# Kernel optimization log

Hardware: AMD Instinct MI355X
Metric: run time of the kernel (lower is better)

Reference implementation:

```python
import jax, jax.numpy as jnp
import numpy as np

DIM = 1024
DIM_HEAD = 64
HEADS = 16
BATCH = 2
SEQ = 2048
SCALE = DIM_HEAD ** -0.5


def setup_inputs() -> dict:
    key = jax.random.key(0)
    ks = jax.random.split(key, 5)
    tokens = jax.random.normal(ks[0], (BATCH, SEQ, DIM), dtype=jnp.float32)
    wq = jax.random.normal(ks[1], (HEADS, DIM, DIM_HEAD), dtype=jnp.float32)
    wk = jax.random.normal(ks[2], (HEADS, DIM, DIM_HEAD), dtype=jnp.float32)
    wv = jax.random.normal(ks[3], (HEADS, DIM, DIM_HEAD), dtype=jnp.float32)
    wo = jax.random.normal(ks[4], (HEADS, DIM_HEAD, DIM), dtype=jnp.float32)
    return {"tokens": tokens, "wq": wq, "wk": wk, "wv": wv, "wo": wo}


def reference(tokens, wq, wk, wv, wo):
    # q, k, v: [b, h, n, dh]
    q = jnp.einsum('bnd,hde->bhne', tokens, wq) * SCALE
    k = jnp.einsum('bnd,hde->bhne', tokens, wk)
    v = jnp.einsum('bnd,hde->bhne', tokens, wv)
    sim = jnp.einsum('bhie,bhje->bhij', q, k)          # [b, h, n, n]
    attn = jax.nn.softmax(sim, axis=-1)
    aggregated = jnp.einsum('bhij,bhje->bhie', attn, v)  # [b, h, n, dh]
    retrieved = jnp.einsum('bhne,hed->bnd', aggregated, wo)  # sum over heads
    return retrieved
```

## Files before the change

kernel.cpp:

```cpp
#include <hip/hip_runtime.h>
#include <hip/hip_fp16.h>
#include <stdint.h>

#define BB 2
#define HH 16
#define SS 2048
#define DD 1024
#define DHH 64
#define QSCALE 0.18033688011112042f

typedef _Float16 half8 __attribute__((ext_vector_type(8)));
typedef _Float16 half4 __attribute__((ext_vector_type(4)));
typedef __fp16 fp16x2 __attribute__((ext_vector_type(2)));
typedef float floatx4 __attribute__((ext_vector_type(4)));

__device__ __forceinline__ floatx4 mfma16(half8 a, half8 b, floatx4 c) {
  return __builtin_amdgcn_mfma_f32_16x16x32_f16(a, b, c, 0, 0, 0);
}

__device__ __forceinline__ void dma16(const _Float16* g, _Float16* l) {
  __builtin_amdgcn_global_load_lds(
      (const __attribute__((address_space(1))) uint32_t*)g,
      (__attribute__((address_space(3))) uint32_t*)l,
      16, 0, 0);
}


__global__ __launch_bounds__(256) void convert_kernel(
    const float* __restrict__ wq, const float* __restrict__ wk,
    const float* __restrict__ wv, const float* __restrict__ wo,
    _Float16* __restrict__ Wh, _Float16* __restrict__ Wl,
    _Float16* __restrict__ Wot)
{
  __shared__ float St[64][68];
  const int kt = blockIdx.x;
  const int hy = blockIdx.y;
  const int z  = blockIdx.z;
  const int t  = (int)threadIdx.x;
  const int k0 = kt * 64;

  const float* src = (z == 0) ? (wq + hy * (DD * DHH))
                   : (z == 1) ? (wk + hy * (DD * DHH))
                   : (z == 2) ? (wv + hy * (DD * DHH))
                   : wo;

  const int rr = t >> 4, cc = (t & 15) * 4;
  if (z < 3) {
    #pragma unroll
    for (int i = 0; i < 4; ++i)
      *(floatx4*)&St[rr + 16 * i][cc] =
          *(const floatx4*)(src + (k0 + rr + 16 * i) * DHH + cc);
  } else {
    const int d0 = hy * 64;
    #pragma unroll
    for (int i = 0; i < 4; ++i)
      *(floatx4*)&St[rr + 16 * i][cc] =
          *(const floatx4*)(src + (k0 + rr + 16 * i) * 1024 + d0 + cc);
  }
  __syncthreads();

  const int e = t >> 2, kc = (t & 3) * 16;
  if (z < 3) {
    const int n = z * 1024 + hy * 64 + e;
    half8 hi0, hi1, lo0, lo1;
    #pragma unroll
    for (int u = 0; u < 16; ++u) {
      float x = St[kc + u][e];
      _Float16 hh = (_Float16)x;
      _Float16 ll = (_Float16)(x - (float)hh);
      if (u < 8) { hi0[u] = hh; lo0[u] = ll; }
      else       { hi1[u - 8] = hh; lo1[u - 8] = ll; }
    }
    *(half8*)(Wh + n * 1024 + k0 + kc)     = hi0;
    *(half8*)(Wh + n * 1024 + k0 + kc + 8) = hi1;
    *(half8*)(Wl + n * 1024 + k0 + kc)     = lo0;
    *(half8*)(Wl + n * 1024 + k0 + kc + 8) = lo1;
  } else {
    const int d0 = hy * 64;
    half8 hi0, hi1;
    #pragma unroll
    for (int u = 0; u < 16; ++u) {
      _Float16 hh = (_Float16)St[kc + u][e];
      if (u < 8) hi0[u] = hh; else hi1[u - 8] = hh;
    }
    *(half8*)(Wot + (d0 + e) * 1024 + k0 + kc)     = hi0;
    *(half8*)(Wot + (d0 + e) * 1024 + k0 + kc + 8) = hi1;
  }
}

__global__ __launch_bounds__(256) void tokens_split_kernel(
    const float* __restrict__ tokens,
    _Float16* __restrict__ th, _Float16* __restrict__ tl)
{
  const int i = ((int)blockIdx.x * 256 + (int)threadIdx.x) * 8;
  floatx4 x0 = *(const floatx4*)(tokens + i);
  floatx4 x1 = *(const floatx4*)(tokens + i + 4);
  half8 h, l;
  #pragma unroll
  for (int j = 0; j < 8; ++j) {
    float x = (j < 4) ? x0[j] : x1[j - 4];
    _Float16 hh = (_Float16)x;
    h[j] = hh;
    l[j] = (_Float16)(x - (float)hh);
  }
  *(half8*)(th + i) = h;
  *(half8*)(tl + i) = l;
}

__global__ __launch_bounds__(256) void qkv_gemm_kernel(
    const _Float16* __restrict__ th, const _Float16* __restrict__ tl,
    const _Float16* __restrict__ Wh, const _Float16* __restrict__ Wl,
    _Float16* __restrict__ qh, _Float16* __restrict__ ql,
    _Float16* __restrict__ kh, _Float16* __restrict__ kl,
    _Float16* __restrict__ vt)
{
  __shared__ alignas(16) _Float16 sbuf[2][4][128 * 32];

  const int n0 = blockIdx.x * 128;
  const int m0 = blockIdx.y * 128;
  const int zb = n0 >> 10;
  const bool is_v = (zb == 2);
  const int t = (int)threadIdx.x;
  const int lane = t & 63, wid = t >> 6;
  const int l16 = lane & 15, q4 = lane >> 4;
  const int mw = (wid & 1) * 64, nw = (wid >> 1) * 64;

  const int g  = (lane & 7) ^ ((lane >> 3) & 7);
  const int grow  = (lane >> 3) * 2 + (g >> 2);
  const int gcol8 = (g & 3) * 8;
  const int laneoff = (l16 >> 1) * 128 + (((((l16 & 1) << 2) | q4) ^ (l16 >> 1)) * 16);

  const _Float16* src;
  int arr;
  if (wid == 0)      { src = th + m0 * 1024; arr = 0; }
  else if (wid == 1) { src = Wh + n0 * 1024; arr = 1; }
  else if (wid == 2) { src = Wl + n0 * 1024; arr = 2; }
  else               { src = tl + m0 * 1024; arr = 3; }
  const bool stage_active = !(is_v && wid == 3);
  const _Float16* gsrc = src + grow * 1024 + gcol8;

  const floatx4 z4 = {0.0f, 0.0f, 0.0f, 0.0f};
  floatx4 acc[4][4];
  #pragma unroll
  for (int mi = 0; mi < 4; ++mi)
    #pragma unroll
    for (int ni = 0; ni < 4; ++ni) acc[mi][ni] = z4;

  auto stage = [&](int buf, int kt2) {
    if (stage_active) {
      const _Float16* gp = gsrc + kt2 * 32;
      _Float16* dst = &sbuf[buf][arr][0];
      #pragma unroll
      for (int j = 0; j < 8; ++j)
        dma16(gp + j * 16 * 1024, dst + j * 16 * 32);
    }
  };

  auto compute = [&](int buf) {
    const char* sAh = (const char*)&sbuf[buf][0][0];
    const char* sBh = (const char*)&sbuf[buf][1][0];
    const char* sBl = (const char*)&sbuf[buf][2][0];
    const char* sAl = (const char*)&sbuf[buf][3][0];
    half8 a_h[4];
    #pragma unroll
    for (int mi = 0; mi < 4; ++mi)
      a_h[mi] = *(const half8*)(sAh + (mw + mi * 16) * 64 + laneoff);
    if (!is_v) {
      half8 a_l[4];
      #pragma unroll
      for (int mi = 0; mi < 4; ++mi)
        a_l[mi] = *(const half8*)(sAl + (mw + mi * 16) * 64 + laneoff);
      #pragma unroll
      for (int ni = 0; ni < 4; ++ni) {
        const half8 b_h = *(const half8*)(sBh + (nw + ni * 16) * 64 + laneoff);
        const half8 b_l = *(const half8*)(sBl + (nw + ni * 16) * 64 + laneoff);
        #pragma unroll
        for (int mi = 0; mi < 4; ++mi) {
          acc[mi][ni] = mfma16(a_h[mi], b_h, acc[mi][ni]);
          acc[mi][ni] = mfma16(a_h[mi], b_l, acc[mi][ni]);
          acc[mi][ni] = mfma16(a_l[mi], b_h, acc[mi][ni]);
        }
      }
    } else {
      #pragma unroll
      for (int ni = 0; ni < 4; ++ni) {
        const half8 b_h = *(const half8*)(sBh + (nw + ni * 16) * 64 + laneoff);
        const half8 b_l = *(const half8*)(sBl + (nw + ni * 16) * 64 + laneoff);
        #pragma unroll
        for (int mi = 0; mi < 4; ++mi) {
          acc[mi][ni] = mfma16(a_h[mi], b_h, acc[mi][ni]);
          acc[mi][ni] = mfma16(a_h[mi], b_l, acc[mi][ni]);
        }
      }
    }
  };

  stage(0, 0);
  __syncthreads();

  #pragma unroll 1
  for (int kt = 0; kt < 32; kt += 2) {
    if (kt + 1 < 32) stage(1, kt + 1);
    compute(0);
    __syncthreads();
    if (kt + 2 < 32) stage(0, kt + 2);
    compute(1);
    __syncthreads();
  }

  #pragma unroll
  for (int ni = 0; ni < 4; ++ni) {
    const int ncol = n0 + nw + ni * 16;
    const int h = (ncol >> 6) & 15;
    const int e = (ncol & 63) + l16;
    #pragma unroll
    for (int mi = 0; mi < 4; ++mi) {
      #pragma unroll
      for (int r = 0; r < 4; ++r) {
        const int grow2 = m0 + mw + mi * 16 + q4 * 4 + r;
        const int b = grow2 >> 11, s = grow2 & 2047;
        const float v = acc[mi][ni][r];
        const int qkidx = ((b * HH + h) * SS + s) * DHH + e;
        if (zb == 0) {
          const float vs = v * QSCALE;
          const _Float16 hh = (_Float16)vs;
          qh[qkidx] = hh;
          ql[qkidx] = (_Float16)(vs - (float)hh);
        } else if (zb == 1) {
          const _Float16 hh = (_Float16)v;
          kh[qkidx] = hh;
          kl[qkidx] = (_Float16)(v - (float)hh);
        } else {
          vt[((b * HH + h) * DHH + e) * SS + s] = (_Float16)v;
        }
      }
    }
  }
}

__global__ __launch_bounds__(512) void attn_kernel(
    const _Float16* __restrict__ qh, const _Float16* __restrict__ ql,
    const _Float16* __restrict__ kh, const _Float16* __restrict__ kl,
    const _Float16* __restrict__ vt, _Float16* __restrict__ agg)
{
  __shared__ _Float16 Kh[64][72], Kl[64][72], Vs[64][72];
  __shared__ _Float16 Ps[128][72];

  const int qt = blockIdx.x;
  const int h  = blockIdx.y;
  const int b  = blockIdx.z;
  const int bh = b * HH + h;
  const int t = (int)threadIdx.x;
  const int lane = t & 63, wid = t >> 6;
  const int l16 = lane & 15, q4 = lane >> 4;

  const int sr = t >> 3, sc = (t & 7) * 8;

  half8 qfh[2], qfl[2];
  {
    const int s = qt * 128 + wid * 16 + l16;
    const int base = (bh * SS + s) * DHH + q4 * 8;
    qfh[0] = *(const half8*)(qh + base);
    qfh[1] = *(const half8*)(qh + base + 32);
    qfl[0] = *(const half8*)(ql + base);
    qfl[1] = *(const half8*)(ql + base + 32);
  }

  const floatx4 z4 = {0.0f, 0.0f, 0.0f, 0.0f};
  floatx4 o[4];
  #pragma unroll
  for (int i = 0; i < 4; ++i) o[i] = z4;
  float m_r = -1e30f, l_r = 0.0f;

  half8 pK, pL, pV;
  {
    const int gk = (bh * SS + sr) * DHH + sc;
    pK = *(const half8*)(kh + gk);
    pL = *(const half8*)(kl + gk);
    pV = *(const half8*)(vt + (bh * DHH + sr) * SS + sc);
  }

  for (int kt = 0; kt < 32; ++kt) {
    __syncthreads();
    *(half8*)&Kh[sr][sc] = pK;
    *(half8*)&Kl[sr][sc] = pL;
    *(half8*)&Vs[sr][sc] = pV;
    __syncthreads();

    if (kt < 31) {
      const int k1 = (kt + 1) * 64;
      const int gk = (bh * SS + k1 + sr) * DHH + sc;
      pK = *(const half8*)(kh + gk);
      pL = *(const half8*)(kl + gk);
      pV = *(const half8*)(vt + (bh * DHH + sr) * SS + k1 + sc);
    }

    floatx4 sv[4];
    #pragma unroll
    for (int sub = 0; sub < 4; ++sub) {
      const half8 ah0 = *(const half8*)&Kh[sub * 16 + l16][q4 * 8];
      const half8 ah1 = *(const half8*)&Kh[sub * 16 + l16][q4 * 8 + 32];
      const half8 al0 = *(const half8*)&Kl[sub * 16 + l16][q4 * 8];
      const half8 al1 = *(const half8*)&Kl[sub * 16 + l16][q4 * 8 + 32];
      floatx4 s4 = z4;
      s4 = mfma16(ah0, qfh[0], s4);
      s4 = mfma16(ah1, qfh[1], s4);
      s4 = mfma16(al0, qfh[0], s4);
      s4 = mfma16(al1, qfh[1], s4);
      s4 = mfma16(ah0, qfl[0], s4);
      s4 = mfma16(ah1, qfl[1], s4);
      sv[sub] = s4;
    }

    float mx = fmaxf(fmaxf(sv[0][0], sv[0][1]), fmaxf(sv[0][2], sv[0][3]));
    #pragma unroll
    for (int sub = 1; sub < 4; ++sub)
      mx = fmaxf(mx, fmaxf(fmaxf(sv[sub][0], sv[sub][1]),
                           fmaxf(sv[sub][2], sv[sub][3])));
    mx = fmaxf(mx, __shfl_xor(mx, 16));
    mx = fmaxf(mx, __shfl_xor(mx, 32));
    const float mnew = fmaxf(m_r, mx);

    float psum = 0.0f;
    #pragma unroll
    for (int sub = 0; sub < 4; ++sub) {
      #pragma unroll
      for (int r = 0; r < 4; ++r) {
        float p = exp2f(sv[sub][r] - mnew);
        sv[sub][r] = p;
        psum += p;
      }
    }

    #pragma unroll
    for (int sub = 0; sub < 4; ++sub) {
      fp16x2 p01 = __builtin_amdgcn_cvt_pkrtz(sv[sub][0], sv[sub][1]);
      fp16x2 p23 = __builtin_amdgcn_cvt_pkrtz(sv[sub][2], sv[sub][3]);
      half4 pv;
      pv[0] = (_Float16)p01[0]; pv[1] = (_Float16)p01[1];
      pv[2] = (_Float16)p23[0]; pv[3] = (_Float16)p23[1];
      *(half4*)&Ps[wid * 16 + l16][sub * 16 + q4 * 4] = pv;
    }

    psum += __shfl_xor(psum, 16);
    psum += __shfl_xor(psum, 32);

    if (__any(mnew > m_r)) {
      const float alpha = exp2f(m_r - mnew);
      l_r = l_r * alpha + psum;
      m_r = mnew;
      #pragma unroll
      for (int sub = 0; sub < 4; ++sub)
        #pragma unroll
        for (int r = 0; r < 4; ++r) o[sub][r] *= alpha;
    } else {
      l_r += psum;
    }

    asm volatile("s_waitcnt lgkmcnt(0)" ::: "memory");

    const half8 pb0 = *(const half8*)&Ps[wid * 16 + l16][q4 * 8];
    const half8 pb1 = *(const half8*)&Ps[wid * 16 + l16][q4 * 8 + 32];
    #pragma unroll
    for (int sub = 0; sub < 4; ++sub) {
      const half8 va0 = *(const half8*)&Vs[sub * 16 + l16][q4 * 8];
      const half8 va1 = *(const half8*)&Vs[sub * 16 + l16][q4 * 8 + 32];
      o[sub] = mfma16(va0, pb0, o[sub]);
      o[sub] = mfma16(va1, pb1, o[sub]);
    }
  }

  const float inv = 1.0f / l_r;
  const int s = qt * 128 + wid * 16 + l16;
  #pragma unroll
  for (int sub = 0; sub < 4; ++sub) {
    half4 ov;
    #pragma unroll
    for (int r = 0; r < 4; ++r) ov[r] = (_Float16)(o[sub][r] * inv);
    *(half4*)(agg + (b * SS + s) * (HH * DHH) + h * DHH + sub * 16 + q4 * 4) = ov;
  }
}

__global__ __launch_bounds__(256) void out_gemm_kernel(
    const _Float16* __restrict__ agg, const _Float16* __restrict__ Wot,
    float* __restrict__ out)
{
  __shared__ alignas(16) _Float16 sbuf[2][2][128 * 32];
  const int n0 = blockIdx.x * 128;
  const int m0 = blockIdx.y * 128;
  const int t = (int)threadIdx.x;
  const int lane = t & 63, wid = t >> 6;
  const int l16 = lane & 15, q4 = lane >> 4;
  const int mw = (wid & 1) * 64, nw = (wid >> 1) * 64;

  const int g  = (lane & 7) ^ ((lane >> 3) & 7);
  const int grow  = (lane >> 3) * 2 + (g >> 2);
  const int gcol8 = (g & 3) * 8;
  const int laneoff = (l16 >> 1) * 128 + (((((l16 & 1) << 2) | q4) ^ (l16 >> 1)) * 16);

  const int arr = wid >> 1;
  const int half64 = (wid & 1) * 64;
  const _Float16* src = (arr == 0) ? (agg + m0 * 1024) : (Wot + n0 * 1024);
  const _Float16* gsrc = src + (half64 + grow) * 1024 + gcol8;

  const floatx4 z4 = {0.0f, 0.0f, 0.0f, 0.0f};
  floatx4 acc[4][4];
  #pragma unroll
  for (int mi = 0; mi < 4; ++mi)
    #pragma unroll
    for (int ni = 0; ni < 4; ++ni) acc[mi][ni] = z4;

  auto stage = [&](int buf, int kt2) {
    const _Float16* gp = gsrc + kt2 * 32;
    _Float16* dst = &sbuf[buf][arr][half64 * 32];
    #pragma unroll
    for (int j = 0; j < 4; ++j)
      dma16(gp + j * 16 * 1024, dst + j * 16 * 32);
  };

  auto compute = [&](int buf) {
    const char* sA = (const char*)&sbuf[buf][0][0];
    const char* sB = (const char*)&sbuf[buf][1][0];
    half8 a_f[4];
    #pragma unroll
    for (int mi = 0; mi < 4; ++mi)
      a_f[mi] = *(const half8*)(sA + (mw + mi * 16) * 64 + laneoff);
    #pragma unroll
    for (int ni = 0; ni < 4; ++ni) {
      const half8 b_f = *(const half8*)(sB + (nw + ni * 16) * 64 + laneoff);
      #pragma unroll
      for (int mi = 0; mi < 4; ++mi)
        acc[mi][ni] = mfma16(a_f[mi], b_f, acc[mi][ni]);
    }
  };

  stage(0, 0);
  __syncthreads();

  #pragma unroll 1
  for (int kt = 0; kt < 32; kt += 2) {
    if (kt + 1 < 32) stage(1, kt + 1);
    compute(0);
    __syncthreads();
    if (kt + 2 < 32) stage(0, kt + 2);
    compute(1);
    __syncthreads();
  }

  #pragma unroll
  for (int ni = 0; ni < 4; ++ni)
    #pragma unroll
    for (int mi = 0; mi < 4; ++mi)
      #pragma unroll
      for (int r = 0; r < 4; ++r)
        out[(m0 + mw + mi * 16 + q4 * 4 + r) * 1024 + n0 + nw + ni * 16 + l16] =
            acc[mi][ni][r];
}

extern "C" void kernel_launch(void* const* d_in, const int* in_sizes, int n_in,
                              void* d_out, int out_size, void* d_ws, size_t ws_size,
                              hipStream_t stream)
{
  const float* tokens = (const float*)d_in[0];
  const float* wq = (const float*)d_in[1];
  const float* wk = (const float*)d_in[2];
  const float* wv = (const float*)d_in[3];
  const float* wo = (const float*)d_in[4];
  float* out = (float*)d_out;

  char* ws = (char*)d_ws;
  _Float16* qh  = (_Float16*)(ws);
  _Float16* ql  = (_Float16*)(ws + 8388608);
  _Float16* kh  = (_Float16*)(ws + 16777216);
  _Float16* kl  = (_Float16*)(ws + 25165824);
  _Float16* vt  = (_Float16*)(ws + 33554432);
  _Float16* Wh  = (_Float16*)(ws + 41943040);
  _Float16* Wl  = (_Float16*)(ws + 48234496);
  _Float16* Wot = (_Float16*)(ws + 54525952);
  _Float16* th  = (_Float16*)(ws + 56623104);
  _Float16* tl  = (_Float16*)(ws + 65011712);
  _Float16* agg = (_Float16*)(ws + 56623104);

  convert_kernel<<<dim3(16, 16, 4), 256, 0, stream>>>(wq, wk, wv, wo, Wh, Wl, Wot);
  tokens_split_kernel<<<2048, 256, 0, stream>>>(tokens, th, tl);
  qkv_gemm_kernel<<<dim3(24, 32), 256, 0, stream>>>(th, tl, Wh, Wl, qh, ql, kh, kl, vt);
  attn_kernel<<<dim3(16, 16, 2), 512, 0, stream>>>(qh, ql, kh, kl, vt, agg);
  out_gemm_kernel<<<dim3(8, 32), 256, 0, stream>>>(agg, Wot, out);
}
```

Baseline: 281.0 us.

## Process two query sub-tiles per wave in attention, add lazy rescale and setprio

The attention kernel now runs 256 threads per block, and each wave handles 32 query rows as two 16-row sub-tiles, so each K/V fragment read from LDS feeds twice as many MFMAs. The online-softmax max is updated only when the new max exceeds the running one by more than 8 (in log2 units), which skips most output rescales. MFMA sections are wrapped in s_setprio. In exchange there are more registers per thread, fewer waves per block, and each thread does twice the K/V staging loads.

```diff
diff --git a/kernel.cpp b/kernel.cpp
--- a/kernel.cpp
+++ b/kernel.cpp
@@ -238,7 +238,7 @@
   }
 }
 
-__global__ __launch_bounds__(512) void attn_kernel(
+__global__ __launch_bounds__(256) void attn_kernel(
     const _Float16* __restrict__ qh, const _Float16* __restrict__ ql,
     const _Float16* __restrict__ kh, const _Float16* __restrict__ kl,
     const _Float16* __restrict__ vt, _Float16* __restrict__ agg)
@@ -254,130 +254,167 @@
   const int lane = t & 63, wid = t >> 6;
   const int l16 = lane & 15, q4 = lane >> 4;
 
-  const int sr = t >> 3, sc = (t & 7) * 8;
-
-  half8 qfh[2], qfl[2];
-  {
-    const int s = qt * 128 + wid * 16 + l16;
+  const int sr = t >> 2, sc = (t & 3) * 16;
+
+  half8 qfh[2][2], qfl[2][2];
+  #pragma unroll
+  for (int u = 0; u < 2; ++u) {
+    const int s = qt * 128 + wid * 32 + u * 16 + l16;
     const int base = (bh * SS + s) * DHH + q4 * 8;
-    qfh[0] = *(const half8*)(qh + base);
-    qfh[1] = *(const half8*)(qh + base + 32);
-    qfl[0] = *(const half8*)(ql + base);
-    qfl[1] = *(const half8*)(ql + base + 32);
+    qfh[u][0] = *(const half8*)(qh + base);
+    qfh[u][1] = *(const half8*)(qh + base + 32);
+    qfl[u][0] = *(const half8*)(ql + base);
+    qfl[u][1] = *(const half8*)(ql + base + 32);
   }
 
   const floatx4 z4 = {0.0f, 0.0f, 0.0f, 0.0f};
-  floatx4 o[4];
-  #pragma unroll
-  for (int i = 0; i < 4; ++i) o[i] = z4;
-  float m_r = -1e30f, l_r = 0.0f;
-
-  half8 pK, pL, pV;
+  floatx4 o[2][4];
+  #pragma unroll
+  for (int u = 0; u < 2; ++u)
+    #pragma unroll
+    for (int i = 0; i < 4; ++i) o[u][i] = z4;
+  float m_r[2] = {-1e30f, -1e30f}, l_r[2] = {0.0f, 0.0f};
+
+  half8 pK0, pK1, pL0, pL1, pV0, pV1;
   {
     const int gk = (bh * SS + sr) * DHH + sc;
-    pK = *(const half8*)(kh + gk);
-    pL = *(const half8*)(kl + gk);
-    pV = *(const half8*)(vt + (bh * DHH + sr) * SS + sc);
+    pK0 = *(const half8*)(kh + gk);
+    pK1 = *(const half8*)(kh + gk + 8);
+    pL0 = *(const half8*)(kl + gk);
+    pL1 = *(const half8*)(kl + gk + 8);
+    const int gv = (bh * DHH + sr) * SS + sc;
+    pV0 = *(const half8*)(vt + gv);
+    pV1 = *(const half8*)(vt + gv + 8);
   }
 
   for (int kt = 0; kt < 32; ++kt) {
     __syncthreads();
-    *(half8*)&Kh[sr][sc] = pK;
-    *(half8*)&Kl[sr][sc] = pL;
-    *(half8*)&Vs[sr][sc] = pV;
+    *(half8*)&Kh[sr][sc]     = pK0;
+    *(half8*)&Kh[sr][sc + 8] = pK1;
+    *(half8*)&Kl[sr][sc]     = pL0;
+    *(half8*)&Kl[sr][sc + 8] = pL1;
+    *(half8*)&Vs[sr][sc]     = pV0;
+    *(half8*)&Vs[sr][sc + 8] = pV1;
     __syncthreads();
 
     if (kt < 31) {
       const int k1 = (kt + 1) * 64;
       const int gk = (bh * SS + k1 + sr) * DHH + sc;
-      pK = *(const half8*)(kh + gk);
-      pL = *(const half8*)(kl + gk);
-      pV = *(const half8*)(vt + (bh * DHH + sr) * SS + k1 + sc);
-    }
-
-    floatx4 sv[4];
+      pK0 = *(const half8*)(kh + gk);
+      pK1 = *(const half8*)(kh + gk + 8);
+      pL0 = *(const half8*)(kl + gk);
+      pL1 = *(const half8*)(kl + gk + 8);
+      const int gv = (bh * DHH + sr) * SS + k1 + sc;
+      pV0 = *(const half8*)(vt + gv);
+      pV1 = *(const half8*)(vt + gv + 8);
+    }
+
+    floatx4 sv[2][4];
+    __builtin_amdgcn_s_setprio(1);
     #pragma unroll
     for (int sub = 0; sub < 4; ++sub) {
       const half8 ah0 = *(const half8*)&Kh[sub * 16 + l16][q4 * 8];
       const half8 ah1 = *(const half8*)&Kh[sub * 16 + l16][q4 * 8 + 32];
       const half8 al0 = *(const half8*)&Kl[sub * 16 + l16][q4 * 8];
       const half8 al1 = *(const half8*)&Kl[sub * 16 + l16][q4 * 8 + 32];
-      floatx4 s4 = z4;
-      s4 = mfma16(ah0, qfh[0], s4);
-      s4 = mfma16(ah1, qfh[1], s4);
-      s4 = mfma16(al0, qfh[0], s4);
-      s4 = mfma16(al1, qfh[1], s4);
-      s4 = mfma16(ah0, qfl[0], s4);
-      s4 = mfma16(ah1, qfl[1], s4);
-      sv[sub] = s4;
-    }
-
-    float mx = fmaxf(fmaxf(sv[0][0], sv[0][1]), fmaxf(sv[0][2], sv[0][3]));
-    #pragma unroll
-    for (int sub = 1; sub < 4; ++sub)
-      mx = fmaxf(mx, fmaxf(fmaxf(sv[sub][0], sv[sub][1]),
-                           fmaxf(sv[sub][2], sv[sub][3])));
-    mx = fmaxf(mx, __shfl_xor(mx, 16));
-    mx = fmaxf(mx, __shfl_xor(mx, 32));
-    const float mnew = fmaxf(m_r, mx);
-
-    float psum = 0.0f;
-    #pragma unroll
-    for (int sub = 0; sub < 4; ++sub) {
-      #pragma unroll
-      for (int r = 0; r < 4; ++r) {
-        float p = exp2f(sv[sub][r] - mnew);
-        sv[sub][r] = p;
-        psum += p;
-      }
-    }
-
-    #pragma unroll
-    for (int sub = 0; sub < 4; ++sub) {
-      fp16x2 p01 = __builtin_amdgcn_cvt_pkrtz(sv[sub][0], sv[sub][1]);
-      fp16x2 p23 = __builtin_amdgcn_cvt_pkrtz(sv[sub][2], sv[sub][3]);
-      half4 pv;
-      pv[0] = (_Float16)p01[0]; pv[1] = (_Float16)p01[1];
-      pv[2] = (_Float16)p23[0]; pv[3] = (_Float16)p23[1];
-      *(half4*)&Ps[wid * 16 + l16][sub * 16 + q4 * 4] = pv;
-    }
-
-    psum += __shfl_xor(psum, 16);
-    psum += __shfl_xor(psum, 32);
-
-    if (__any(mnew > m_r)) {
-      const float alpha = exp2f(m_r - mnew);
-      l_r = l_r * alpha + psum;
-      m_r = mnew;
-      #pragma unroll
-      for (int sub = 0; sub < 4; ++sub)
+      #pragma unroll
+      for (int u = 0; u < 2; ++u) {
+        floatx4 s4 = z4;
+        s4 = mfma16(ah0, qfh[u][0], s4);
+        s4 = mfma16(ah1, qfh[u][1], s4);
+        s4 = mfma16(al0, qfh[u][0], s4);
+        s4 = mfma16(al1, qfh[u][1], s4);
+        s4 = mfma16(ah0, qfl[u][0], s4);
+        s4 = mfma16(ah1, qfl[u][1], s4);
+        sv[u][sub] = s4;
+      }
+    }
+    __builtin_amdgcn_s_setprio(0);
+
+    #pragma unroll
+    for (int u = 0; u < 2; ++u) {
+      float mx = fmaxf(fmaxf(sv[u][0][0], sv[u][0][1]),
+                       fmaxf(sv[u][0][2], sv[u][0][3]));
+      #pragma unroll
+      for (int sub = 1; sub < 4; ++sub)
+        mx = fmaxf(mx, fmaxf(fmaxf(sv[u][sub][0], sv[u][sub][1]),
+                             fmaxf(sv[u][sub][2], sv[u][sub][3])));
+      mx = fmaxf(mx, __shfl_xor(mx, 16));
+      mx = fmaxf(mx, __shfl_xor(mx, 32));
+
+      const bool need = __any(mx > m_r[u] + 8.0f);
+      const float mnew = need ? fmaxf(m_r[u], mx) : m_r[u];
+
+      float psum = 0.0f;
+      #pragma unroll
+      for (int sub = 0; sub < 4; ++sub) {
         #pragma unroll
-        for (int r = 0; r < 4; ++r) o[sub][r] *= alpha;
-    } else {
-      l_r += psum;
+        for (int r = 0; r < 4; ++r) {
+          float p = exp2f(sv[u][sub][r] - mnew);
+          sv[u][sub][r] = p;
+          psum += p;
+        }
+      }
+
+      #pragma unroll
+      for (int sub = 0; sub < 4; ++sub) {
+        fp16x2 p01 = __builtin_amdgcn_cvt_pkrtz(sv[u][sub][0], sv[u][sub][1]);
+        fp16x2 p23 = __builtin_amdgcn_cvt_pkrtz(sv[u][sub][2], sv[u][sub][3]);
+        half4 pv;
+        pv[0] = (_Float16)p01[0]; pv[1] = (_Float16)p01[1];
+        pv[2] = (_Float16)p23[0]; pv[3] = (_Float16)p23[1];
+        *(half4*)&Ps[wid * 32 + u * 16 + l16][sub * 16 + q4 * 4] = pv;
+      }
+
+      psum += __shfl_xor(psum, 16);
+      psum += __shfl_xor(psum, 32);
+
+      if (need) {
+        const float alpha = exp2f(m_r[u] - mnew);
+        l_r[u] = l_r[u] * alpha + psum;
+        m_r[u] = mnew;
+        #pragma unroll
+        for (int sub = 0; sub < 4; ++sub)
+          #pragma unroll
+          for (int r = 0; r < 4; ++r) o[u][sub][r] *= alpha;
+      } else {
+        l_r[u] += psum;
+      }
     }
 
     asm volatile("s_waitcnt lgkmcnt(0)" ::: "memory");
 
-    const half8 pb0 = *(const half8*)&Ps[wid * 16 + l16][q4 * 8];
-    const half8 pb1 = *(const half8*)&Ps[wid * 16 + l16][q4 * 8 + 32];
+    half8 pb0[2], pb1[2];
+    #pragma unroll
+    for (int u = 0; u < 2; ++u) {
+      pb0[u] = *(const half8*)&Ps[wid * 32 + u * 16 + l16][q4 * 8];
+      pb1[u] = *(const half8*)&Ps[wid * 32 + u * 16 + l16][q4 * 8 + 32];
+    }
+    __builtin_amdgcn_s_setprio(1);
     #pragma unroll
     for (int sub = 0; sub < 4; ++sub) {
       const half8 va0 = *(const half8*)&Vs[sub * 16 + l16][q4 * 8];
       const half8 va1 = *(const half8*)&Vs[sub * 16 + l16][q4 * 8 + 32];
-      o[sub] = mfma16(va0, pb0, o[sub]);
-      o[sub] = mfma16(va1, pb1, o[sub]);
-    }
-  }
-
-  const float inv = 1.0f / l_r;
-  const int s = qt * 128 + wid * 16 + l16;
-  #pragma unroll
-  for (int sub = 0; sub < 4; ++sub) {
-    half4 ov;
-    #pragma unroll
-    for (int r = 0; r < 4; ++r) ov[r] = (_Float16)(o[sub][r] * inv);
-    *(half4*)(agg + (b * SS + s) * (HH * DHH) + h * DHH + sub * 16 + q4 * 4) = ov;
+      #pragma unroll
+      for (int u = 0; u < 2; ++u) {
+        o[u][sub] = mfma16(va0, pb0[u], o[u][sub]);
+        o[u][sub] = mfma16(va1, pb1[u], o[u][sub]);
+      }
+    }
+    __builtin_amdgcn_s_setprio(0);
+  }
+
+  #pragma unroll
+  for (int u = 0; u < 2; ++u) {
+    const float inv = 1.0f / l_r[u];
+    const int s = qt * 128 + wid * 32 + u * 16 + l16;
+    #pragma unroll
+    for (int sub = 0; sub < 4; ++sub) {
+      half4 ov;
+      #pragma unroll
+      for (int r = 0; r < 4; ++r) ov[r] = (_Float16)(o[u][sub][r] * inv);
+      *(half4*)(agg + (b * SS + s) * (HH * DHH) + h * DHH + sub * 16 + q4 * 4) = ov;
+    }
   }
 }
 
@@ -484,6 +521,6 @@
   convert_kernel<<<dim3(16, 16, 4), 256, 0, stream>>>(wq, wk, wv, wo, Wh, Wl, Wot);
   tokens_split_kernel<<<2048, 256, 0, stream>>>(tokens, th, tl);
   qkv_gemm_kernel<<<dim3(24, 32), 256, 0, stream>>>(th, tl, Wh, Wl, qh, ql, kh, kl, vt);
-  attn_kernel<<<dim3(16, 16, 2), 512, 0, stream>>>(qh, ql, kh, kl, vt, agg);
+  attn_kernel<<<dim3(16, 16, 2), 256, 0, stream>>>(qh, ql, kh, kl, vt, agg);
   out_gemm_kernel<<<dim3(8, 32), 256, 0, stream>>>(agg, Wot, out);
 }
```

Result: no change. 277.4 us (-1.3%).

## Keep P in registers, lazy softmax rescale, double-buffer K/V LDS

Applied to the files above, without the earlier changes.

The attention loop now feeds the exponentiated scores straight from registers into 16x16x16 MFMAs, so the Ps shared-memory round trip and its waitcnt go away. The running max is updated only when some lane's tile max exceeds the stored max by more than 8 (log2 units). The row sum is kept per lane and reduced once at the end instead of every tile. K/V shared tiles are double-buffered so one barrier per iteration is enough, and s_setprio raises wave priority around the MFMA sections. The lazy rescale lets unnormalised probabilities grow up to 2^8 before fp16 conversion, which trades some headroom and precision for fewer reductions and shuffles.

```diff
diff --git a/kernel.cpp b/kernel.cpp
--- a/kernel.cpp
+++ b/kernel.cpp
@@ -17,6 +17,9 @@
 __device__ __forceinline__ floatx4 mfma16(half8 a, half8 b, floatx4 c) {
   return __builtin_amdgcn_mfma_f32_16x16x32_f16(a, b, c, 0, 0, 0);
 }
+__device__ __forceinline__ floatx4 mfma16k16(half4 a, half4 b, floatx4 c) {
+  return __builtin_amdgcn_mfma_f32_16x16x16f16(a, b, c, 0, 0, 0);
+}
 
 __device__ __forceinline__ void dma16(const _Float16* g, _Float16* l) {
   __builtin_amdgcn_global_load_lds(
@@ -24,7 +27,6 @@
       (__attribute__((address_space(3))) uint32_t*)l,
       16, 0, 0);
 }
-
 
 __global__ __launch_bounds__(256) void convert_kernel(
     const float* __restrict__ wq, const float* __restrict__ wk,
@@ -243,8 +245,7 @@
     const _Float16* __restrict__ kh, const _Float16* __restrict__ kl,
     const _Float16* __restrict__ vt, _Float16* __restrict__ agg)
 {
-  __shared__ _Float16 Kh[64][72], Kl[64][72], Vs[64][72];
-  __shared__ _Float16 Ps[128][72];
+  __shared__ _Float16 Kh[2][64][72], Kl[2][64][72], Vs[2][64][72];
 
   const int qt = blockIdx.x;
   const int h  = blockIdx.y;
@@ -270,7 +271,8 @@
   floatx4 o[4];
   #pragma unroll
   for (int i = 0; i < 4; ++i) o[i] = z4;
-  float m_r = -1e30f, l_r = 0.0f;
+  float m_r = -1e30f;
+  float l_lane = 0.0f;
 
   half8 pK, pL, pV;
   {
@@ -280,11 +282,10 @@
     pV = *(const half8*)(vt + (bh * DHH + sr) * SS + sc);
   }
 
-  for (int kt = 0; kt < 32; ++kt) {
-    __syncthreads();
-    *(half8*)&Kh[sr][sc] = pK;
-    *(half8*)&Kl[sr][sc] = pL;
-    *(half8*)&Vs[sr][sc] = pV;
+  auto body = [&](int buf, int kt) {
+    *(half8*)&Kh[buf][sr][sc] = pK;
+    *(half8*)&Kl[buf][sr][sc] = pL;
+    *(half8*)&Vs[buf][sr][sc] = pV;
     __syncthreads();
 
     if (kt < 31) {
@@ -296,12 +297,13 @@
     }
 
     floatx4 sv[4];
+    __builtin_amdgcn_s_setprio(1);
     #pragma unroll
     for (int sub = 0; sub < 4; ++sub) {
-      const half8 ah0 = *(const half8*)&Kh[sub * 16 + l16][q4 * 8];
-      const half8 ah1 = *(const half8*)&Kh[sub * 16 + l16][q4 * 8 + 32];
-      const half8 al0 = *(const half8*)&Kl[sub * 16 + l16][q4 * 8];
-      const half8 al1 = *(const half8*)&Kl[sub * 16 + l16][q4 * 8 + 32];
+      const half8 ah0 = *(const half8*)&Kh[buf][sub * 16 + l16][q4 * 8];
+      const half8 ah1 = *(const half8*)&Kh[buf][sub * 16 + l16][q4 * 8 + 32];
+      const half8 al0 = *(const half8*)&Kl[buf][sub * 16 + l16][q4 * 8];
+      const half8 al1 = *(const half8*)&Kl[buf][sub * 16 + l16][q4 * 8 + 32];
       floatx4 s4 = z4;
       s4 = mfma16(ah0, qfh[0], s4);
       s4 = mfma16(ah1, qfh[1], s4);
@@ -311,66 +313,66 @@
       s4 = mfma16(ah1, qfl[1], s4);
       sv[sub] = s4;
     }
-
-    float mx = fmaxf(fmaxf(sv[0][0], sv[0][1]), fmaxf(sv[0][2], sv[0][3]));
-    #pragma unroll
-    for (int sub = 1; sub < 4; ++sub)
-      mx = fmaxf(mx, fmaxf(fmaxf(sv[sub][0], sv[sub][1]),
-                           fmaxf(sv[sub][2], sv[sub][3])));
-    mx = fmaxf(mx, __shfl_xor(mx, 16));
-    mx = fmaxf(mx, __shfl_xor(mx, 32));
-    const float mnew = fmaxf(m_r, mx);
-
-    float psum = 0.0f;
-    #pragma unroll
-    for (int sub = 0; sub < 4; ++sub) {
-      #pragma unroll
-      for (int r = 0; r < 4; ++r) {
-        float p = exp2f(sv[sub][r] - mnew);
-        sv[sub][r] = p;
-        psum += p;
-      }
-    }
-
-    #pragma unroll
-    for (int sub = 0; sub < 4; ++sub) {
-      fp16x2 p01 = __builtin_amdgcn_cvt_pkrtz(sv[sub][0], sv[sub][1]);
-      fp16x2 p23 = __builtin_amdgcn_cvt_pkrtz(sv[sub][2], sv[sub][3]);
-      half4 pv;
-      pv[0] = (_Float16)p01[0]; pv[1] = (_Float16)p01[1];
-      pv[2] = (_Float16)p23[0]; pv[3] = (_Float16)p23[1];
-      *(half4*)&Ps[wid * 16 + l16][sub * 16 + q4 * 4] = pv;
-    }
-
-    psum += __shfl_xor(psum, 16);
-    psum += __shfl_xor(psum, 32);
-
-    if (__any(mnew > m_r)) {
+    __builtin_amdgcn_s_setprio(0);
+
+    float m0 = fmaxf(fmaxf(sv[0][0], sv[0][1]), fmaxf(sv[0][2], sv[0][3]));
+    float m1 = fmaxf(fmaxf(sv[1][0], sv[1][1]), fmaxf(sv[1][2], sv[1][3]));
+    float m2 = fmaxf(fmaxf(sv[2][0], sv[2][1]), fmaxf(sv[2][2], sv[2][3]));
+    float m3 = fmaxf(fmaxf(sv[3][0], sv[3][1]), fmaxf(sv[3][2], sv[3][3]));
+    const float mx = fmaxf(fmaxf(m0, m1), fmaxf(m2, m3));
+
+    if (__any(mx > m_r + 8.0f)) {
+      float mc = fmaxf(mx, __shfl_xor(mx, 16));
+      mc = fmaxf(mc, __shfl_xor(mc, 32));
+      const float mnew = fmaxf(m_r, mc);
       const float alpha = exp2f(m_r - mnew);
-      l_r = l_r * alpha + psum;
       m_r = mnew;
+      l_lane *= alpha;
       #pragma unroll
       for (int sub = 0; sub < 4; ++sub)
         #pragma unroll
         for (int r = 0; r < 4; ++r) o[sub][r] *= alpha;
-    } else {
-      l_r += psum;
-    }
-
-    asm volatile("s_waitcnt lgkmcnt(0)" ::: "memory");
-
-    const half8 pb0 = *(const half8*)&Ps[wid * 16 + l16][q4 * 8];
-    const half8 pb1 = *(const half8*)&Ps[wid * 16 + l16][q4 * 8 + 32];
-    #pragma unroll
-    for (int sub = 0; sub < 4; ++sub) {
-      const half8 va0 = *(const half8*)&Vs[sub * 16 + l16][q4 * 8];
-      const half8 va1 = *(const half8*)&Vs[sub * 16 + l16][q4 * 8 + 32];
-      o[sub] = mfma16(va0, pb0, o[sub]);
-      o[sub] = mfma16(va1, pb1, o[sub]);
-    }
-  }
-
-  const float inv = 1.0f / l_r;
+    }
+
+    half4 p4[4];
+    #pragma unroll
+    for (int c = 0; c < 4; ++c) {
+      const float p0 = exp2f(sv[c][0] - m_r);
+      const float p1 = exp2f(sv[c][1] - m_r);
+      const float p2 = exp2f(sv[c][2] - m_r);
+      const float p3 = exp2f(sv[c][3] - m_r);
+      l_lane += (p0 + p1) + (p2 + p3);
+      const fp16x2 a01 = __builtin_amdgcn_cvt_pkrtz(p0, p1);
+      const fp16x2 a23 = __builtin_amdgcn_cvt_pkrtz(p2, p3);
+      half4 pv;
+      pv[0] = (_Float16)a01[0]; pv[1] = (_Float16)a01[1];
+      pv[2] = (_Float16)a23[0]; pv[3] = (_Float16)a23[1];
+      p4[c] = pv;
+    }
+
+    __builtin_amdgcn_s_setprio(1);
+    #pragma unroll
+    for (int c = 0; c < 4; ++c) {
+      #pragma unroll
+      for (int sub = 0; sub < 4; ++sub) {
+        const half4 va =
+            *(const half4*)&Vs[buf][sub * 16 + l16][c * 16 + q4 * 4];
+        o[sub] = mfma16k16(va, p4[c], o[sub]);
+      }
+    }
+    __builtin_amdgcn_s_setprio(0);
+  };
+
+  #pragma unroll 1
+  for (int kt = 0; kt < 32; kt += 2) {
+    body(0, kt);
+    body(1, kt + 1);
+  }
+
+  float lsum = l_lane;
+  lsum += __shfl_xor(lsum, 16);
+  lsum += __shfl_xor(lsum, 32);
+  const float inv = 1.0f / lsum;
   const int s = qt * 128 + wid * 16 + l16;
   #pragma unroll
   for (int sub = 0; sub < 4; ++sub) {
```

After: 284.0 us. No clear change (+1.1%).
